# Kernel optimization log

Hardware: AMD Instinct MI355X
Metric: run time of the kernel (lower is better)

## Reference

```python
import jax, jax.numpy as jnp
import numpy as np

B, L, D_MODEL, N_HEAD, D_K, D_V, VOCAB = 2, 1024, 512, 8, 64, 64, 64
TEMP = float(np.sqrt(D_K))
LN_EPS = 1e-5


def setup_inputs() -> dict:
    key = jax.random.key(0)
    ks = jax.random.split(key, 24)
    inp = {}
    inp['q'] = jax.random.normal(ks[0], (B, L, D_MODEL), jnp.float32)
    inp['k'] = jax.random.normal(ks[1], (B, L, D_MODEL), jnp.float32)
    inp['v'] = jax.random.normal(ks[2], (B, L, D_MODEL), jnp.float32)
    inp['mask'] = jax.random.uniform(ks[3], (B, L, L)) < 0.1
    # tf_f1 carries -1 (padding) positions; its sign defines tf_mask for ALL five features
    inp['tf_f1'] = jax.random.randint(ks[4], (B, L, L), -1, VOCAB, jnp.int32)
    inp['tf_f2'] = jax.random.randint(ks[5], (B, L, L), 0, VOCAB, jnp.int32)
    inp['tf_f3'] = jax.random.randint(ks[6], (B, L, L), 0, VOCAB, jnp.int32)
    inp['tf_f4'] = jax.random.randint(ks[7], (B, L, L), 0, VOCAB, jnp.int32)
    inp['tf_f5'] = jax.random.randint(ks[8], (B, L, L), 0, VOCAB, jnp.int32)
    s_qk = np.sqrt(2.0 / (D_MODEL + D_K))
    s_v = np.sqrt(2.0 / (D_MODEL + D_V))
    inp['w_q'] = jax.random.normal(ks[9], (D_MODEL, N_HEAD * D_K), jnp.float32) * s_qk
    inp['b_q'] = jnp.zeros((N_HEAD * D_K,), jnp.float32)
    inp['w_k'] = jax.random.normal(ks[10], (D_MODEL, N_HEAD * D_K), jnp.float32) * s_qk
    inp['b_k'] = jnp.zeros((N_HEAD * D_K,), jnp.float32)
    inp['w_v'] = jax.random.normal(ks[11], (D_MODEL, N_HEAD * D_V), jnp.float32) * s_v
    inp['b_v'] = jnp.zeros((N_HEAD * D_V,), jnp.float32)
    for i in range(5):
        inp[f'emb{i+1}'] = jax.random.normal(ks[12 + i], (VOCAB, N_HEAD), jnp.float32)
    fc_std = np.sqrt(2.0 / (N_HEAD * D_V + D_MODEL))
    inp['fc_w'] = jax.random.normal(ks[17], (N_HEAD * D_V, D_MODEL), jnp.float32) * fc_std
    inp['fc_b'] = jnp.zeros((D_MODEL,), jnp.float32)
    inp['ln_g'] = jnp.ones((D_MODEL,), jnp.float32)
    inp['ln_b'] = jnp.zeros((D_MODEL,), jnp.float32)
    return inp


def _bias(emb, tf, tf_mask):
    # (tf * mask).long() embedding lookup, zeroed where mask==0 -> [H, B, L, L]
    idx = (tf.astype(jnp.float32) * tf_mask).astype(jnp.int32)
    feat = emb[idx] * tf_mask[..., None]          # [B, L, L, H]
    return jnp.transpose(feat, (3, 0, 1, 2))      # [H, B, L, L]


def reference(q, k, v, mask, tf_f1, tf_f2, tf_f3, tf_f4, tf_f5,
              w_q, b_q, w_k, b_k, w_v, b_v,
              emb1, emb2, emb3, emb4, emb5,
              fc_w, fc_b, ln_g, ln_b):
    residual = q
    qh = (q @ w_q + b_q).reshape(B, L, N_HEAD, D_K)
    kh = (k @ w_k + b_k).reshape(B, L, N_HEAD, D_K)
    vh = (v @ w_v + b_v).reshape(B, L, N_HEAD, D_V)

    scores = jnp.einsum('blhd,bmhd->hblm', qh, kh)  # [H, B, Lq, Lk]
    tf_mask = (tf_f1 >= 0).astype(jnp.float32)      # [B, L, L] (from tf_f1 only, as in torch)
    scores = (scores
              + _bias(emb1, tf_f1, tf_mask)
              + _bias(emb2, tf_f2, tf_mask)
              + _bias(emb3, tf_f3, tf_mask)
              + _bias(emb4, tf_f4, tf_mask)
              + _bias(emb5, tf_f5, tf_mask)) / TEMP
    scores = jnp.where(mask[None], -jnp.inf, scores)
    attn = jax.nn.softmax(scores, axis=-1)          # [H, B, L, L]; dropout = identity (eval)

    out = jnp.einsum('hblm,bmhd->blhd', attn, vh).reshape(B, L, N_HEAD * D_V)
    out = out @ fc_w + fc_b                          # dropout = identity (eval)
    out = out + residual
    mu = jnp.mean(out, axis=-1, keepdims=True)
    var = jnp.mean((out - mu) ** 2, axis=-1, keepdims=True)
    out = (out - mu) * jax.lax.rsqrt(var + LN_EPS) * ln_g + ln_b
    return out, attn.reshape(N_HEAD * B, L, L)
```

## Files before the change

kernel.cpp:

```cpp
#include <hip/hip_runtime.h>
#include <math.h>

#define L_SEQ 1024
#define DMODEL 512
#define NHEAD 8
#define NB 2

typedef __attribute__((ext_vector_type(8))) short bf8;
typedef __attribute__((ext_vector_type(4))) float f4;

__device__ __forceinline__ short f2bf(float f) {
    unsigned u = __float_as_uint(f);
    unsigned r = u + 0x7FFF + ((u >> 16) & 1);
    return (short)(r >> 16);
}

__global__ __launch_bounds__(256) void cast_bf16_kernel(
    const float* __restrict__ src, short* __restrict__ dst, int n4)
{
    int i = blockIdx.x * 256 + threadIdx.x;
    if (i < n4) {
        float4 f = ((const float4*)src)[i];
        short4 o;
        o.x = f2bf(f.x); o.y = f2bf(f.y); o.z = f2bf(f.z); o.w = f2bf(f.w);
        ((short4*)dst)[i] = o;
    }
}

__global__ __launch_bounds__(256) void transpose_cast_kernel(
    const float* __restrict__ s0, const float* __restrict__ s1,
    const float* __restrict__ s2, const float* __restrict__ s3,
    short* __restrict__ d0, short* __restrict__ d1,
    short* __restrict__ d2, short* __restrict__ d3)
{
    const float* src; short* dst;
    switch (blockIdx.z) {
        case 0: src = s0; dst = d0; break;
        case 1: src = s1; dst = d1; break;
        case 2: src = s2; dst = d2; break;
        default: src = s3; dst = d3; break;
    }
    __shared__ float tile[32][33];
    const int tx = threadIdx.x, ty = threadIdx.y;
    const int x0 = blockIdx.x * 32, y0 = blockIdx.y * 32;
#pragma unroll
    for (int j = 0; j < 32; j += 8)
        tile[ty + j][tx] = src[(size_t)(y0 + ty + j) * 512 + x0 + tx];
    __syncthreads();
#pragma unroll
    for (int j = 0; j < 32; j += 8)
        dst[(size_t)(x0 + ty + j) * 512 + y0 + tx] = f2bf(tile[tx][ty + j]);
}

template<int MODE>
__global__ __launch_bounds__(256) void gemm_mfma_kernel(
    const short* __restrict__ A, const short* __restrict__ Bt,
    const float* __restrict__ bias, void* __restrict__ Cout)
{
    const int w = threadIdx.x >> 6, lane = threadIdx.x & 63;
    const int lr = lane & 15, lq = lane >> 4;
    const int m_base = blockIdx.y * 64 + w * 16;
    const int n_base = blockIdx.x * 64;

    f4 acc[4];
    const f4 zero = {0.f, 0.f, 0.f, 0.f};
#pragma unroll
    for (int nf = 0; nf < 4; ++nf) acc[nf] = zero;

    for (int k0 = 0; k0 < 512; k0 += 32) {
        bf8 a = *(const bf8*)(A + (size_t)(m_base + lr) * 512 + k0 + lq * 8);
#pragma unroll
        for (int nf = 0; nf < 4; ++nf) {
            bf8 b = *(const bf8*)(Bt + (size_t)(n_base + nf * 16 + lr) * 512 + k0 + lq * 8);
            acc[nf] = __builtin_amdgcn_mfma_f32_16x16x32_bf16(a, b, acc[nf], 0, 0, 0);
        }
    }

#pragma unroll
    for (int nf = 0; nf < 4; ++nf) {
        const int n = n_base + nf * 16 + lr;
        const float bv = bias[n];
        const int mrow = m_base + lq * 4;
#pragma unroll
        for (int r = 0; r < 4; ++r) {
            const float val = acc[nf][r] + bv;
            const int m = mrow + r;
            if (MODE == 0) {
                ((short*)Cout)[(size_t)m * 512 + n] = f2bf(val);
            } else if (MODE == 1) {
                const int bb = m >> 10, l = m & 1023;
                ((short*)Cout)[((size_t)bb * 512 + n) * 1024 + l] = f2bf(val);
            } else {
                ((float*)Cout)[(size_t)m * 512 + n] = val;
            }
        }
    }
}

__global__ __launch_bounds__(256) void scores_mfma_kernel(
    const short* __restrict__ qh, const short* __restrict__ kh,
    float* __restrict__ sc)
{
    const int z = blockIdx.z, h = z >> 1, b = z & 1;
    const int w = threadIdx.x >> 6, lane = threadIdx.x & 63;
    const int wr = w >> 1, wc = w & 1;
    const int lr = lane & 15, lq = lane >> 4;
    const int l0 = blockIdx.y * 128 + wr * 64;
    const int m0 = blockIdx.x * 128 + wc * 64;
    const int colb = h * 64 + lq * 8;
    const size_t base = (size_t)b * L_SEQ * DMODEL;

    bf8 afr[4][2], bfr[4][2];
#pragma unroll
    for (int i = 0; i < 4; ++i)
#pragma unroll
        for (int kk = 0; kk < 2; ++kk) {
            afr[i][kk] = *(const bf8*)(qh + base + (size_t)(l0 + i * 16 + lr) * 512 + colb + kk * 32);
            bfr[i][kk] = *(const bf8*)(kh + base + (size_t)(m0 + i * 16 + lr) * 512 + colb + kk * 32);
        }

    f4 acc[4][4];
    const f4 zero = {0.f, 0.f, 0.f, 0.f};
#pragma unroll
    for (int mt = 0; mt < 4; ++mt)
#pragma unroll
        for (int nt = 0; nt < 4; ++nt) acc[mt][nt] = zero;

#pragma unroll
    for (int kk = 0; kk < 2; ++kk)
#pragma unroll
        for (int mt = 0; mt < 4; ++mt)
#pragma unroll
            for (int nt = 0; nt < 4; ++nt)
                acc[mt][nt] = __builtin_amdgcn_mfma_f32_16x16x32_bf16(
                    afr[mt][kk], bfr[nt][kk], acc[mt][nt], 0, 0, 0);

    float* out = sc + (size_t)z * L_SEQ * L_SEQ;
#pragma unroll
    for (int mt = 0; mt < 4; ++mt)
#pragma unroll
        for (int nt = 0; nt < 4; ++nt)
#pragma unroll
            for (int r = 0; r < 4; ++r)
                out[(size_t)(l0 + mt * 16 + lq * 4 + r) * 1024 + m0 + nt * 16 + lr] = acc[mt][nt][r];
}

__global__ __launch_bounds__(256, 4) void bias_softmax_kernel(
    float* __restrict__ attn,
    const int* __restrict__ mask,
    const int* __restrict__ tf1, const int* __restrict__ tf2,
    const int* __restrict__ tf3, const int* __restrict__ tf4,
    const int* __restrict__ tf5,
    const float* __restrict__ emb1, const float* __restrict__ emb2,
    const float* __restrict__ emb3, const float* __restrict__ emb4,
    const float* __restrict__ emb5)
{
    const int l = blockIdx.x, b = blockIdx.y, t = threadIdx.x;
    __shared__ float embs[5][NHEAD][64];
    __shared__ float redmx[4][NHEAD];
    __shared__ float redsm[4][NHEAD];

    {
        const float* es[5] = {emb1, emb2, emb3, emb4, emb5};
#pragma unroll
        for (int it = 0; it < 10; ++it) {
            const int i = it * 256 + t;
            const int j = it >> 1;
            const int rem = i & 511;
            const int h = rem >> 6, idx = rem & 63;
            embs[j][h][idx] = es[j][idx * NHEAD + h];
        }
    }
    __syncthreads();

    const size_t rowbase = ((size_t)(b * L_SEQ + l)) * L_SEQ + (size_t)(t * 4);
    const int4 mk  = *(const int4*)(mask + rowbase);
    const int4 i1v = *(const int4*)(tf1 + rowbase);
    const int4 i2v = *(const int4*)(tf2 + rowbase);
    const int4 i3v = *(const int4*)(tf3 + rowbase);
    const int4 i4v = *(const int4*)(tf4 + rowbase);
    const int4 i5v = *(const int4*)(tf5 + rowbase);

    f4 av[NHEAD];
#pragma unroll
    for (int h = 0; h < NHEAD; ++h)
        av[h] = *(const f4*)(attn + ((size_t)(h * NB + b) * L_SEQ + l) * L_SEQ + t * 4);

#define BIAS_FOLD(MI, I1, I2, I3, I4, I5, MK)                                   \
    {                                                                           \
        const float tfm = ((I1) >= 0) ? 1.0f : 0.0f;                            \
        const int c1 = ((I1) >= 0) ? (I1) : 0;                                  \
        _Pragma("unroll")                                                       \
        for (int h = 0; h < NHEAD; ++h) {                                       \
            const float bsum = embs[0][h][c1] + embs[1][h][I2]                  \
                             + embs[2][h][I3] + embs[3][h][I4]                  \
                             + embs[4][h][I5];                                  \
            av[h][MI] = (MK) ? -INFINITY                                        \
                             : (av[h][MI] + bsum * tfm) * 0.125f;               \
        }                                                                       \
    }

    BIAS_FOLD(0, i1v.x, i2v.x, i3v.x, i4v.x, i5v.x, mk.x)
    BIAS_FOLD(1, i1v.y, i2v.y, i3v.y, i4v.y, i5v.y, mk.y)
    BIAS_FOLD(2, i1v.z, i2v.z, i3v.z, i4v.z, i5v.z, mk.z)
    BIAS_FOLD(3, i1v.w, i2v.w, i3v.w, i4v.w, i5v.w, mk.w)
#undef BIAS_FOLD

    const int wid = t >> 6, lane = t & 63;

    float mx[NHEAD];
#pragma unroll
    for (int h = 0; h < NHEAD; ++h)
        mx[h] = fmaxf(fmaxf(av[h][0], av[h][1]), fmaxf(av[h][2], av[h][3]));
#pragma unroll
    for (int h = 0; h < NHEAD; ++h) {
#pragma unroll
        for (int off = 1; off < 64; off <<= 1)
            mx[h] = fmaxf(mx[h], __shfl_xor(mx[h], off));
    }
    if (lane == 0) {
#pragma unroll
        for (int h = 0; h < NHEAD; ++h) redmx[wid][h] = mx[h];
    }
    __syncthreads();
#pragma unroll
    for (int h = 0; h < NHEAD; ++h)
        mx[h] = fmaxf(fmaxf(redmx[0][h], redmx[1][h]),
                      fmaxf(redmx[2][h], redmx[3][h]));

    float sm[NHEAD];
#pragma unroll
    for (int h = 0; h < NHEAD; ++h) {
        f4 e;
        e[0] = __expf(av[h][0] - mx[h]);
        e[1] = __expf(av[h][1] - mx[h]);
        e[2] = __expf(av[h][2] - mx[h]);
        e[3] = __expf(av[h][3] - mx[h]);
        av[h] = e;
        sm[h] = (e[0] + e[1]) + (e[2] + e[3]);
    }
#pragma unroll
    for (int h = 0; h < NHEAD; ++h) {
#pragma unroll
        for (int off = 1; off < 64; off <<= 1)
            sm[h] += __shfl_xor(sm[h], off);
    }
    if (lane == 0) {
#pragma unroll
        for (int h = 0; h < NHEAD; ++h) redsm[wid][h] = sm[h];
    }
    __syncthreads();

#pragma unroll
    for (int h = 0; h < NHEAD; ++h) {
        const float tot = (redsm[0][h] + redsm[1][h]) + (redsm[2][h] + redsm[3][h]);
        const float inv = 1.0f / tot;
        f4 o = av[h] * inv;
        *(f4*)(attn + ((size_t)(h * NB + b) * L_SEQ + l) * L_SEQ + t * 4) = o;
    }
}

__global__ __launch_bounds__(256) void av_mfma_kernel(
    const float* __restrict__ attn, const short* __restrict__ vht,
    short* __restrict__ pv)
{
    const int z = blockIdx.y, h = z >> 1, b = z & 1;
    const int w = threadIdx.x >> 6, lane = threadIdx.x & 63;
    const int lr = lane & 15, lq = lane >> 4;
    const int l0 = blockIdx.x * 128 + w * 32;
    const float* Ab = attn + (size_t)z * L_SEQ * L_SEQ;
    const short* Bb = vht + ((size_t)b * 512 + h * 64) * 1024;

    f4 acc[2][4];
    const f4 zero = {0.f, 0.f, 0.f, 0.f};
#pragma unroll
    for (int mt = 0; mt < 2; ++mt)
#pragma unroll
        for (int nt = 0; nt < 4; ++nt) acc[mt][nt] = zero;

    for (int k0 = 0; k0 < L_SEQ; k0 += 32) {
        bf8 a[2];
#pragma unroll
        for (int mt = 0; mt < 2; ++mt) {
            const float* p = Ab + (size_t)(l0 + mt * 16 + lr) * 1024 + k0 + lq * 8;
            float4 f0 = *(const float4*)p;
            float4 f1 = *(const float4*)(p + 4);
            bf8 tv;
            tv[0] = f2bf(f0.x); tv[1] = f2bf(f0.y); tv[2] = f2bf(f0.z); tv[3] = f2bf(f0.w);
            tv[4] = f2bf(f1.x); tv[5] = f2bf(f1.y); tv[6] = f2bf(f1.z); tv[7] = f2bf(f1.w);
            a[mt] = tv;
        }
#pragma unroll
        for (int nt = 0; nt < 4; ++nt) {
            bf8 bv = *(const bf8*)(Bb + (size_t)(nt * 16 + lr) * 1024 + k0 + lq * 8);
            acc[0][nt] = __builtin_amdgcn_mfma_f32_16x16x32_bf16(a[0], bv, acc[0][nt], 0, 0, 0);
            acc[1][nt] = __builtin_amdgcn_mfma_f32_16x16x32_bf16(a[1], bv, acc[1][nt], 0, 0, 0);
        }
    }

#pragma unroll
    for (int nt = 0; nt < 4; ++nt) {
        const int n = nt * 16 + lr;
#pragma unroll
        for (int mt = 0; mt < 2; ++mt) {
            const int rowb = l0 + mt * 16 + lq * 4;
#pragma unroll
            for (int r = 0; r < 4; ++r)
                pv[(size_t)(b * L_SEQ + rowb + r) * 512 + h * 64 + n] = f2bf(acc[mt][nt][r]);
        }
    }
}

__global__ __launch_bounds__(256) void ln_kernel(
    const float* __restrict__ x, const float* __restrict__ res,
    const float* __restrict__ g, const float* __restrict__ bvec,
    float* __restrict__ out)
{
    const int row = blockIdx.x;
    const int t = threadIdx.x;
    float2 xv = ((const float2*)(x + (size_t)row * DMODEL))[t];
    float2 rv = ((const float2*)(res + (size_t)row * DMODEL))[t];
    const float a = xv.x + rv.x;
    const float c = xv.y + rv.y;
    float s = a + c, sq = a * a + c * c;
#pragma unroll
    for (int off = 32; off; off >>= 1) {
        s  += __shfl_down(s, off);
        sq += __shfl_down(sq, off);
    }
    __shared__ float ssum[4], ssq[4];
    __shared__ float smu, srs;
    const int wid = t >> 6, lane = t & 63;
    if (lane == 0) { ssum[wid] = s; ssq[wid] = sq; }
    __syncthreads();
    if (t == 0) {
        float ts = ssum[0] + ssum[1] + ssum[2] + ssum[3];
        float tq = ssq[0] + ssq[1] + ssq[2] + ssq[3];
        float mu = ts * (1.0f / DMODEL);
        float var = tq * (1.0f / DMODEL) - mu * mu;
        smu = mu;
        srs = rsqrtf(var + 1e-5f);
    }
    __syncthreads();
    const float mu = smu, rs = srs;
    float2 gv = ((const float2*)g)[t];
    float2 bv = ((const float2*)bvec)[t];
    float2 o;
    o.x = (a - mu) * rs * gv.x + bv.x;
    o.y = (c - mu) * rs * gv.y + bv.y;
    ((float2*)(out + (size_t)row * DMODEL))[t] = o;
}

extern "C" void kernel_launch(void* const* d_in, const int* in_sizes, int n_in,
                              void* d_out, int out_size, void* d_ws, size_t ws_size,
                              hipStream_t stream)
{
    const float* q    = (const float*)d_in[0];
    const float* k    = (const float*)d_in[1];
    const float* v    = (const float*)d_in[2];
    const int*   mask = (const int*)d_in[3];
    const int*   tf1  = (const int*)d_in[4];
    const int*   tf2  = (const int*)d_in[5];
    const int*   tf3  = (const int*)d_in[6];
    const int*   tf4  = (const int*)d_in[7];
    const int*   tf5  = (const int*)d_in[8];
    const float* w_q  = (const float*)d_in[9];
    const float* b_q  = (const float*)d_in[10];
    const float* w_k  = (const float*)d_in[11];
    const float* b_k  = (const float*)d_in[12];
    const float* w_v  = (const float*)d_in[13];
    const float* b_v  = (const float*)d_in[14];
    const float* emb1 = (const float*)d_in[15];
    const float* emb2 = (const float*)d_in[16];
    const float* emb3 = (const float*)d_in[17];
    const float* emb4 = (const float*)d_in[18];
    const float* emb5 = (const float*)d_in[19];
    const float* fc_w = (const float*)d_in[20];
    const float* fc_b = (const float*)d_in[21];
    const float* ln_g = (const float*)d_in[22];
    const float* ln_b = (const float*)d_in[23];

    float* out  = (float*)d_out;
    float* attn = out + (size_t)NB * L_SEQ * DMODEL;

    char* wsb = (char*)d_ws;
    short* qb   = (short*)(wsb + 0);
    short* kb   = (short*)(wsb + (2u << 20));
    short* vb   = (short*)(wsb + (4u << 20));
    short* Wtq  = (short*)(wsb + (6u << 20));
    short* Wtk  = (short*)(wsb + (6u << 20) + (512u << 10));
    short* Wtv  = (short*)(wsb + (7u << 20));
    short* Wtfc = (short*)(wsb + (7u << 20) + (512u << 10));
    short* qh   = (short*)(wsb + (8u << 20));
    short* kh   = (short*)(wsb + (10u << 20));
    short* vht  = (short*)(wsb + (12u << 20));
    short* pv   = (short*)(wsb + (14u << 20));
    float* fco  = (float*)(wsb + (16u << 20));

    const int n4 = NB * L_SEQ * DMODEL / 4;

    cast_bf16_kernel<<<n4 / 256, 256, 0, stream>>>(q, qb, n4);
    cast_bf16_kernel<<<n4 / 256, 256, 0, stream>>>(k, kb, n4);
    cast_bf16_kernel<<<n4 / 256, 256, 0, stream>>>(v, vb, n4);

    transpose_cast_kernel<<<dim3(16, 16, 4), dim3(32, 8), 0, stream>>>(
        w_q, w_k, w_v, fc_w, Wtq, Wtk, Wtv, Wtfc);

    dim3 gproj(DMODEL / 64, NB * L_SEQ / 64);
    gemm_mfma_kernel<0><<<gproj, 256, 0, stream>>>(qb, Wtq, b_q, qh);
    gemm_mfma_kernel<0><<<gproj, 256, 0, stream>>>(kb, Wtk, b_k, kh);
    gemm_mfma_kernel<1><<<gproj, 256, 0, stream>>>(vb, Wtv, b_v, vht);

    scores_mfma_kernel<<<dim3(8, 8, 16), 256, 0, stream>>>(qh, kh, attn);

    bias_softmax_kernel<<<dim3(L_SEQ, NB), 256, 0, stream>>>(
        attn, mask, tf1, tf2, tf3, tf4, tf5, emb1, emb2, emb3, emb4, emb5);

    av_mfma_kernel<<<dim3(8, 16), 256, 0, stream>>>(attn, vht, pv);

    gemm_mfma_kernel<2><<<gproj, 256, 0, stream>>>(pv, Wtfc, fc_b, fco);

    ln_kernel<<<NB * L_SEQ, 256, 0, stream>>>(fco, q, ln_g, ln_b, out);
}
```

Measured before the change: 284.7 us.

## Batch cast/projection launches, shrink GEMM tiles, split-K the attention-V kernel

Merges the three input casts into one launch and the three projection GEMMs into one z-indexed launch. Projection and FC GEMMs move to 32x32 tiles with 128 threads so more blocks fill the CUs. The attn@V kernel switches to split-K across 4 waves, with a shared-memory reduction over 16-row tiles, raising grid size from 128 to 1024 blocks. The softmax kernel drops its occupancy hint and issues its global loads before the embedding-table staging so their latency overlaps. Smaller tiles mean less operand reuse per block and extra reduction traffic in exchange for better parallelism.

```diff
diff --git a/kernel.cpp b/kernel.cpp
--- a/kernel.cpp
+++ b/kernel.cpp
@@ -15,9 +15,18 @@
     return (short)(r >> 16);
 }
 
-__global__ __launch_bounds__(256) void cast_bf16_kernel(
-    const float* __restrict__ src, short* __restrict__ dst, int n4)
-{
+__global__ __launch_bounds__(256) void cast3_bf16_kernel(
+    const float* __restrict__ s0, const float* __restrict__ s1,
+    const float* __restrict__ s2,
+    short* __restrict__ d0, short* __restrict__ d1, short* __restrict__ d2,
+    int n4)
+{
+    const float* src; short* dst;
+    switch (blockIdx.y) {
+        case 0: src = s0; dst = d0; break;
+        case 1: src = s1; dst = d1; break;
+        default: src = s2; dst = d2; break;
+    }
     int i = blockIdx.x * 256 + threadIdx.x;
     if (i < n4) {
         float4 f = ((const float4*)src)[i];
@@ -52,32 +61,41 @@
         dst[(size_t)(x0 + ty + j) * 512 + y0 + tx] = f2bf(tile[tx][ty + j]);
 }
 
-template<int MODE>
-__global__ __launch_bounds__(256) void gemm_mfma_kernel(
-    const short* __restrict__ A, const short* __restrict__ Bt,
-    const float* __restrict__ bias, void* __restrict__ Cout)
-{
+__global__ __launch_bounds__(128) void proj_gemm_kernel(
+    const short* __restrict__ qb, const short* __restrict__ kb,
+    const short* __restrict__ vb,
+    const short* __restrict__ Wtq, const short* __restrict__ Wtk,
+    const short* __restrict__ Wtv,
+    const float* __restrict__ b_q, const float* __restrict__ b_k,
+    const float* __restrict__ b_v,
+    short* __restrict__ qh, short* __restrict__ kh, short* __restrict__ vht)
+{
+    const int z = blockIdx.z;
+    const short* A    = (z == 0) ? qb  : (z == 1) ? kb  : vb;
+    const short* Bt   = (z == 0) ? Wtq : (z == 1) ? Wtk : Wtv;
+    const float* bias = (z == 0) ? b_q : (z == 1) ? b_k : b_v;
+
     const int w = threadIdx.x >> 6, lane = threadIdx.x & 63;
     const int lr = lane & 15, lq = lane >> 4;
-    const int m_base = blockIdx.y * 64 + w * 16;
-    const int n_base = blockIdx.x * 64;
-
-    f4 acc[4];
+    const int m_base = blockIdx.y * 32 + w * 16;
+    const int n_base = blockIdx.x * 32;
+
+    f4 acc[2];
     const f4 zero = {0.f, 0.f, 0.f, 0.f};
-#pragma unroll
-    for (int nf = 0; nf < 4; ++nf) acc[nf] = zero;
+    acc[0] = zero; acc[1] = zero;
 
     for (int k0 = 0; k0 < 512; k0 += 32) {
         bf8 a = *(const bf8*)(A + (size_t)(m_base + lr) * 512 + k0 + lq * 8);
 #pragma unroll
-        for (int nf = 0; nf < 4; ++nf) {
+        for (int nf = 0; nf < 2; ++nf) {
             bf8 b = *(const bf8*)(Bt + (size_t)(n_base + nf * 16 + lr) * 512 + k0 + lq * 8);
             acc[nf] = __builtin_amdgcn_mfma_f32_16x16x32_bf16(a, b, acc[nf], 0, 0, 0);
         }
     }
 
-#pragma unroll
-    for (int nf = 0; nf < 4; ++nf) {
+    short* Cnat = (z == 0) ? qh : kh;
+#pragma unroll
+    for (int nf = 0; nf < 2; ++nf) {
         const int n = n_base + nf * 16 + lr;
         const float bv = bias[n];
         const int mrow = m_base + lq * 4;
@@ -85,15 +103,46 @@
         for (int r = 0; r < 4; ++r) {
             const float val = acc[nf][r] + bv;
             const int m = mrow + r;
-            if (MODE == 0) {
-                ((short*)Cout)[(size_t)m * 512 + n] = f2bf(val);
-            } else if (MODE == 1) {
+            if (z < 2) {
+                Cnat[(size_t)m * 512 + n] = f2bf(val);
+            } else {
                 const int bb = m >> 10, l = m & 1023;
-                ((short*)Cout)[((size_t)bb * 512 + n) * 1024 + l] = f2bf(val);
-            } else {
-                ((float*)Cout)[(size_t)m * 512 + n] = val;
+                vht[((size_t)bb * 512 + n) * 1024 + l] = f2bf(val);
             }
         }
+    }
+}
+
+__global__ __launch_bounds__(128) void fc_gemm_kernel(
+    const short* __restrict__ A, const short* __restrict__ Bt,
+    const float* __restrict__ bias, float* __restrict__ Cout)
+{
+    const int w = threadIdx.x >> 6, lane = threadIdx.x & 63;
+    const int lr = lane & 15, lq = lane >> 4;
+    const int m_base = blockIdx.y * 32 + w * 16;
+    const int n_base = blockIdx.x * 32;
+
+    f4 acc[2];
+    const f4 zero = {0.f, 0.f, 0.f, 0.f};
+    acc[0] = zero; acc[1] = zero;
+
+    for (int k0 = 0; k0 < 512; k0 += 32) {
+        bf8 a = *(const bf8*)(A + (size_t)(m_base + lr) * 512 + k0 + lq * 8);
+#pragma unroll
+        for (int nf = 0; nf < 2; ++nf) {
+            bf8 b = *(const bf8*)(Bt + (size_t)(n_base + nf * 16 + lr) * 512 + k0 + lq * 8);
+            acc[nf] = __builtin_amdgcn_mfma_f32_16x16x32_bf16(a, b, acc[nf], 0, 0, 0);
+        }
+    }
+
+#pragma unroll
+    for (int nf = 0; nf < 2; ++nf) {
+        const int n = n_base + nf * 16 + lr;
+        const float bv = bias[n];
+        const int mrow = m_base + lq * 4;
+#pragma unroll
+        for (int r = 0; r < 4; ++r)
+            Cout[(size_t)(mrow + r) * 512 + n] = acc[nf][r] + bv;
     }
 }
 
@@ -145,7 +194,7 @@
                 out[(size_t)(l0 + mt * 16 + lq * 4 + r) * 1024 + m0 + nt * 16 + lr] = acc[mt][nt][r];
 }
 
-__global__ __launch_bounds__(256, 4) void bias_softmax_kernel(
+__global__ __launch_bounds__(256) void bias_softmax_kernel(
     float* __restrict__ attn,
     const int* __restrict__ mask,
     const int* __restrict__ tf1, const int* __restrict__ tf2,
@@ -160,19 +209,6 @@
     __shared__ float redmx[4][NHEAD];
     __shared__ float redsm[4][NHEAD];
 
-    {
-        const float* es[5] = {emb1, emb2, emb3, emb4, emb5};
-#pragma unroll
-        for (int it = 0; it < 10; ++it) {
-            const int i = it * 256 + t;
-            const int j = it >> 1;
-            const int rem = i & 511;
-            const int h = rem >> 6, idx = rem & 63;
-            embs[j][h][idx] = es[j][idx * NHEAD + h];
-        }
-    }
-    __syncthreads();
-
     const size_t rowbase = ((size_t)(b * L_SEQ + l)) * L_SEQ + (size_t)(t * 4);
     const int4 mk  = *(const int4*)(mask + rowbase);
     const int4 i1v = *(const int4*)(tf1 + rowbase);
@@ -185,6 +221,19 @@
 #pragma unroll
     for (int h = 0; h < NHEAD; ++h)
         av[h] = *(const f4*)(attn + ((size_t)(h * NB + b) * L_SEQ + l) * L_SEQ + t * 4);
+
+    {
+        const float* es[5] = {emb1, emb2, emb3, emb4, emb5};
+#pragma unroll
+        for (int it = 0; it < 10; ++it) {
+            const int i = it * 256 + t;
+            const int j = it >> 1;
+            const int rem = i & 511;
+            const int h = rem >> 6, idx = rem & 63;
+            embs[j][h][idx] = es[j][idx * NHEAD + h];
+        }
+    }
+    __syncthreads();
 
 #define BIAS_FOLD(MI, I1, I2, I3, I4, I5, MK)                                   \
     {                                                                           \
@@ -267,48 +316,48 @@
     const int z = blockIdx.y, h = z >> 1, b = z & 1;
     const int w = threadIdx.x >> 6, lane = threadIdx.x & 63;
     const int lr = lane & 15, lq = lane >> 4;
-    const int l0 = blockIdx.x * 128 + w * 32;
+    const int l0 = blockIdx.x * 16;
     const float* Ab = attn + (size_t)z * L_SEQ * L_SEQ;
     const short* Bb = vht + ((size_t)b * 512 + h * 64) * 1024;
 
-    f4 acc[2][4];
+    f4 acc[4];
     const f4 zero = {0.f, 0.f, 0.f, 0.f};
 #pragma unroll
-    for (int mt = 0; mt < 2; ++mt)
-#pragma unroll
-        for (int nt = 0; nt < 4; ++nt) acc[mt][nt] = zero;
-
-    for (int k0 = 0; k0 < L_SEQ; k0 += 32) {
-        bf8 a[2];
-#pragma unroll
-        for (int mt = 0; mt < 2; ++mt) {
-            const float* p = Ab + (size_t)(l0 + mt * 16 + lr) * 1024 + k0 + lq * 8;
-            float4 f0 = *(const float4*)p;
-            float4 f1 = *(const float4*)(p + 4);
-            bf8 tv;
-            tv[0] = f2bf(f0.x); tv[1] = f2bf(f0.y); tv[2] = f2bf(f0.z); tv[3] = f2bf(f0.w);
-            tv[4] = f2bf(f1.x); tv[5] = f2bf(f1.y); tv[6] = f2bf(f1.z); tv[7] = f2bf(f1.w);
-            a[mt] = tv;
-        }
+    for (int nt = 0; nt < 4; ++nt) acc[nt] = zero;
+
+    const int kbeg = w * 256;
+    for (int k0 = kbeg; k0 < kbeg + 256; k0 += 32) {
+        const float* p = Ab + (size_t)(l0 + lr) * 1024 + k0 + lq * 8;
+        float4 f0 = *(const float4*)p;
+        float4 f1 = *(const float4*)(p + 4);
+        bf8 a;
+        a[0] = f2bf(f0.x); a[1] = f2bf(f0.y); a[2] = f2bf(f0.z); a[3] = f2bf(f0.w);
+        a[4] = f2bf(f1.x); a[5] = f2bf(f1.y); a[6] = f2bf(f1.z); a[7] = f2bf(f1.w);
 #pragma unroll
         for (int nt = 0; nt < 4; ++nt) {
             bf8 bv = *(const bf8*)(Bb + (size_t)(nt * 16 + lr) * 1024 + k0 + lq * 8);
-            acc[0][nt] = __builtin_amdgcn_mfma_f32_16x16x32_bf16(a[0], bv, acc[0][nt], 0, 0, 0);
-            acc[1][nt] = __builtin_amdgcn_mfma_f32_16x16x32_bf16(a[1], bv, acc[1][nt], 0, 0, 0);
-        }
-    }
-
-#pragma unroll
-    for (int nt = 0; nt < 4; ++nt) {
-        const int n = nt * 16 + lr;
-#pragma unroll
-        for (int mt = 0; mt < 2; ++mt) {
-            const int rowb = l0 + mt * 16 + lq * 4;
-#pragma unroll
-            for (int r = 0; r < 4; ++r)
-                pv[(size_t)(b * L_SEQ + rowb + r) * 512 + h * 64 + n] = f2bf(acc[mt][nt][r]);
-        }
-    }
+            acc[nt] = __builtin_amdgcn_mfma_f32_16x16x32_bf16(a, bv, acc[nt], 0, 0, 0);
+        }
+    }
+
+    __shared__ float red[4][4][16][17];
+#pragma unroll
+    for (int nt = 0; nt < 4; ++nt)
+#pragma unroll
+        for (int r = 0; r < 4; ++r)
+            red[w][nt][lq * 4 + r][lr] = acc[nt][r];
+    __syncthreads();
+
+    f4 sum = zero;
+#pragma unroll
+    for (int j = 0; j < 4; ++j)
+#pragma unroll
+        for (int r = 0; r < 4; ++r)
+            sum[r] += red[j][w][lq * 4 + r][lr];
+
+#pragma unroll
+    for (int r = 0; r < 4; ++r)
+        pv[(size_t)(b * L_SEQ + l0 + lq * 4 + r) * 512 + h * 64 + w * 16 + lr] = f2bf(sum[r]);
 }
 
 __global__ __launch_bounds__(256) void ln_kernel(
@@ -399,26 +448,23 @@
 
     const int n4 = NB * L_SEQ * DMODEL / 4;
 
-    cast_bf16_kernel<<<n4 / 256, 256, 0, stream>>>(q, qb, n4);
-    cast_bf16_kernel<<<n4 / 256, 256, 0, stream>>>(k, kb, n4);
-    cast_bf16_kernel<<<n4 / 256, 256, 0, stream>>>(v, vb, n4);
+    cast3_bf16_kernel<<<dim3(n4 / 256, 3), 256, 0, stream>>>(
+        q, k, v, qb, kb, vb, n4);
 
     transpose_cast_kernel<<<dim3(16, 16, 4), dim3(32, 8), 0, stream>>>(
         w_q, w_k, w_v, fc_w, Wtq, Wtk, Wtv, Wtfc);
 
-    dim3 gproj(DMODEL / 64, NB * L_SEQ / 64);
-    gemm_mfma_kernel<0><<<gproj, 256, 0, stream>>>(qb, Wtq, b_q, qh);
-    gemm_mfma_kernel<0><<<gproj, 256, 0, stream>>>(kb, Wtk, b_k, kh);
-    gemm_mfma_kernel<1><<<gproj, 256, 0, stream>>>(vb, Wtv, b_v, vht);
+    proj_gemm_kernel<<<dim3(16, 64, 3), 128, 0, stream>>>(
+        qb, kb, vb, Wtq, Wtk, Wtv, b_q, b_k, b_v, qh, kh, vht);
 
     scores_mfma_kernel<<<dim3(8, 8, 16), 256, 0, stream>>>(qh, kh, attn);
 
     bias_softmax_kernel<<<dim3(L_SEQ, NB), 256, 0, stream>>>(
         attn, mask, tf1, tf2, tf3, tf4, tf5, emb1, emb2, emb3, emb4, emb5);
 
-    av_mfma_kernel<<<dim3(8, 16), 256, 0, stream>>>(attn, vht, pv);
-
-    gemm_mfma_kernel<2><<<gproj, 256, 0, stream>>>(pv, Wtfc, fc_b, fco);
+    av_mfma_kernel<<<dim3(64, 16), 256, 0, stream>>>(attn, vht, pv);
+
+    fc_gemm_kernel<<<dim3(16, 64), 128, 0, stream>>>(pv, Wtfc, fc_b, fco);
 
     ln_kernel<<<NB * L_SEQ, 256, 0, stream>>>(fco, q, ln_g, ln_b, out);
 }
```

Result: faster. 274.8 us (-3.5%).
